# Kernel optimization log

Measured on AMD Instinct MI355X. Metric: run time of the kernel, lower is better.

The kernel has to match this reference:

```python
import jax, jax.numpy as jnp
import numpy as np

N = 50000      # nodes
E = 800000     # edges (before self-loops)
DIN = 128      # input feature dim
DOUT = 128     # per-head output dim
H = 4          # heads (concat=False -> mean over heads)
SLOPE = 0.2    # PyG GATConv default negative_slope


def setup_inputs() -> dict:
    key = jax.random.key(0)
    k1, k2, k3, k4, k5 = jax.random.split(key, 5)
    x = jax.random.normal(k1, (N, DIN), dtype=jnp.float32)
    edge_index = jax.random.randint(k2, (2, E), 0, N)
    W = jax.random.normal(k3, (DIN, H * DOUT), dtype=jnp.float32) / np.sqrt(DIN).astype(np.float32)
    att_src = jax.random.normal(k4, (H, DOUT), dtype=jnp.float32) * 0.1
    att_dst = jax.random.normal(k5, (H, DOUT), dtype=jnp.float32) * 0.1
    return {"x": x, "edge_index": edge_index, "W": W, "att_src": att_src, "att_dst": att_dst}


def _gat(x, W, att_src, att_dst, src, dst):
    h = (x @ W).reshape(N, H, DOUT)                      # [N,H,C] shared lin for src/dst
    a_s = jnp.einsum('nhc,hc->nh', h, att_src)           # [N,H]
    a_d = jnp.einsum('nhc,hc->nh', h, att_dst)           # [N,H]
    logits = jax.nn.leaky_relu(a_s[src] + a_d[dst], SLOPE)   # [Etot,H]
    m = jax.ops.segment_max(logits, dst, num_segments=N)     # segment softmax (stable)
    e = jnp.exp(logits - m[dst])
    denom = jax.ops.segment_sum(e, dst, num_segments=N)
    alpha = e / (denom[dst] + 1e-16)                         # [Etot,H]
    out = jax.ops.segment_sum(alpha[:, :, None] * h[src], dst, num_segments=N)  # [N,H,C]
    return out.mean(axis=1)                                   # concat=False -> average heads


def reference(x, edge_index, W, att_src, att_dst):
    loop = jnp.arange(N, dtype=edge_index.dtype)          # add_self_loops=True (PyG default)
    src = jnp.concatenate([edge_index[0], loop])
    dst = jnp.concatenate([edge_index[1], loop])
    return _gat(x, W, att_src, att_dst, src, dst)
```

## Files before the change

kernel.cpp:

```cpp
#include <hip/hip_runtime.h>

#define NN 50000
#define EE 800000
#define ETOT (EE + NN)
#define MAXD 96
#define NBK 196
#define CAP 6144
#define CHX 2304
#define TM 16

typedef _Float16 f16x8 __attribute__((ext_vector_type(8)));
typedef _Float16 f16x2 __attribute__((ext_vector_type(2)));
typedef float f32x4 __attribute__((ext_vector_type(4)));
typedef float f32x2 __attribute__((ext_vector_type(2)));
typedef unsigned int u32x4 __attribute__((ext_vector_type(4)));

__device__ __forceinline__ float lrelu(float v) { return v > 0.f ? v : 0.2f * v; }
__device__ __forceinline__ unsigned int pack2(float a, float b) {
  unsigned short lo = __builtin_bit_cast(unsigned short, (_Float16)a);
  unsigned short hi = __builtin_bit_cast(unsigned short, (_Float16)b);
  return (unsigned int)lo | ((unsigned int)hi << 16);
}

__global__ void k_prep(const float* __restrict__ W,
                       const float* __restrict__ att_s,
                       const float* __restrict__ att_d,
                       unsigned short* __restrict__ Bt,
                       float* __restrict__ WaS, float* __restrict__ WaD,
                       int* __restrict__ bcnt) {
  int gid = blockIdx.x * blockDim.x + threadIdx.x;
  if (gid < NBK) bcnt[gid] = 0;
  if (gid < 128 * 512) {
    int col = gid >> 9, k = gid & 511;
    float v = W[(k & 127) * 512 + (k >> 7) * 128 + col];
    _Float16 hv = (_Float16)v;
    Bt[col * 512 + k] = __builtin_bit_cast(unsigned short, hv);
  }
  if (gid < 512) {
    int k = gid >> 2, h = gid & 3;
    const float* wrow = W + k * 512 + h * 128;
    const float* as = att_s + h * 128;
    const float* ad = att_d + h * 128;
    float ss = 0.f, sd = 0.f;
    for (int c = 0; c < 128; ++c) { float w = wrow[c]; ss += w * as[c]; sd += w * ad[c]; }
    WaS[k * 4 + h] = ss;
    WaD[k * 4 + h] = sd;
  }
}

__global__ __launch_bounds__(256) void k_xcast_p1(const float* __restrict__ x,
                                                  const float* __restrict__ WaS,
                                                  const float* __restrict__ WaD,
                                                  const int* __restrict__ ei,
                                                  unsigned int* __restrict__ xh,
                                                  float* __restrict__ a_s,
                                                  float* __restrict__ a_d,
                                                  int* __restrict__ bcnt,
                                                  unsigned int* __restrict__ ebuf) {
  __shared__ unsigned long long D[128][33];
  __shared__ float4 wsl[128];
  __shared__ float4 wdl[128];
  __shared__ int cnt[NBK];
  __shared__ int gbase[NBK];
  int t = threadIdx.x;
  int nb = blockIdx.x * 128;
  if (t < 128) wsl[t] = ((const float4*)WaS)[t];
  else wdl[t - 128] = ((const float4*)WaD)[t - 128];
  for (int i = t; i < NBK; i += 256) cnt[i] = 0;

#pragma unroll
  for (int i = 0; i < 16; ++i) {
    int idx = t + i * 256;
    int n = idx >> 5, c4 = idx & 31;
    int gn = nb + n;
    float4 v = make_float4(0.f, 0.f, 0.f, 0.f);
    if (gn < NN) v = ((const float4*)x)[(size_t)gn * 32 + c4];
    unsigned int lo = pack2(v.x, v.y);
    unsigned int hi = pack2(v.z, v.w);
    if (gn < NN) ((uint2*)xh)[(size_t)gn * 32 + c4] = make_uint2(lo, hi);
    D[n][c4] = (unsigned long long)lo | ((unsigned long long)hi << 32);
  }
  __syncthreads();

  {
    int n = t >> 1, half = t & 1;
    float s0 = 0.f, s1 = 0.f, s2 = 0.f, s3 = 0.f;
    float d0 = 0.f, d1 = 0.f, d2 = 0.f, d3 = 0.f;
#pragma unroll
    for (int p = 0; p < 16; ++p) {
      int c4 = 2 * p + half;
      unsigned long long q = D[n][c4];
      f16x2 lo2 = __builtin_bit_cast(f16x2, (unsigned int)q);
      f16x2 hi2 = __builtin_bit_cast(f16x2, (unsigned int)(q >> 32));
      float f0 = (float)lo2[0], f1 = (float)lo2[1];
      float f2 = (float)hi2[0], f3 = (float)hi2[1];
      int c = c4 * 4;
      float4 w0 = wsl[c], w1 = wsl[c + 1], w2 = wsl[c + 2], w3 = wsl[c + 3];
      s0 += f0 * w0.x + f1 * w1.x + f2 * w2.x + f3 * w3.x;
      s1 += f0 * w0.y + f1 * w1.y + f2 * w2.y + f3 * w3.y;
      s2 += f0 * w0.z + f1 * w1.z + f2 * w2.z + f3 * w3.z;
      s3 += f0 * w0.w + f1 * w1.w + f2 * w2.w + f3 * w3.w;
      float4 v0 = wdl[c], v1 = wdl[c + 1], v2 = wdl[c + 2], v3 = wdl[c + 3];
      d0 += f0 * v0.x + f1 * v1.x + f2 * v2.x + f3 * v3.x;
      d1 += f0 * v0.y + f1 * v1.y + f2 * v2.y + f3 * v3.y;
      d2 += f0 * v0.z + f1 * v1.z + f2 * v2.z + f3 * v3.z;
      d3 += f0 * v0.w + f1 * v1.w + f2 * v2.w + f3 * v3.w;
    }
    s0 += __shfl_xor(s0, 1); s1 += __shfl_xor(s1, 1);
    s2 += __shfl_xor(s2, 1); s3 += __shfl_xor(s3, 1);
    d0 += __shfl_xor(d0, 1); d1 += __shfl_xor(d1, 1);
    d2 += __shfl_xor(d2, 1); d3 += __shfl_xor(d3, 1);
    int gn = nb + n;
    if (half == 0 && gn < NN) {
      *(float4*)(a_s + gn * 4) = make_float4(s0, s1, s2, s3);
      *(float4*)(a_d + gn * 4) = make_float4(d0, d1, d2, d3);
    }
  }

  int e0 = blockIdx.x * CHX;
#pragma unroll
  for (int k = 0; k < CHX / 256; ++k) {
    int e = e0 + t + k * 256;
    if (e < ETOT) {
      int d = (e < EE) ? ei[EE + e] : (e - EE);
      atomicAdd(&cnt[d >> 8], 1);
    }
  }
  __syncthreads();
  for (int i = t; i < NBK; i += 256) {
    gbase[i] = (cnt[i] > 0) ? atomicAdd(&bcnt[i], cnt[i]) : 0;
    cnt[i] = 0;
  }
  __syncthreads();
#pragma unroll
  for (int k = 0; k < CHX / 256; ++k) {
    int e = e0 + t + k * 256;
    if (e < ETOT) {
      int s, d;
      if (e < EE) { s = ei[e]; d = ei[EE + e]; } else { s = d = e - EE; }
      int b = d >> 8;
      int idx = gbase[b] + atomicAdd(&cnt[b], 1);
      if (idx < CAP)
        ebuf[(size_t)b * CAP + idx] = (unsigned int)s | ((unsigned int)(d & 255) << 16);
    }
  }
}

__global__ __launch_bounds__(256) void k_p2(const unsigned int* __restrict__ ebuf,
                                            const int* __restrict__ bcnt,
                                            int* __restrict__ rs,
                                            unsigned short* __restrict__ perm16) {
  __shared__ int sb[256];
  __shared__ int loc[256];
  __shared__ int cnt[256];
  __shared__ unsigned short out16[CAP];
  __shared__ int basesh;
  int b = blockIdx.x, t = threadIdx.x;

  int v = (t < NBK) ? bcnt[t] : 0;
  sb[t] = v;
  __syncthreads();
  for (int off = 1; off < 256; off <<= 1) {
    int u = (t >= off) ? sb[t - off] : 0;
    __syncthreads();
    sb[t] += u;
    __syncthreads();
  }
  if (t == b) basesh = sb[t] - v;
  cnt[t] = 0;
  __syncthreads();

  int base = basesh;
  int m = min(bcnt[b], CAP);
  int d0 = b * 256;
  const unsigned int* rec = ebuf + (size_t)b * CAP;
  for (int i = t; i < m; i += 256) atomicAdd(&cnt[rec[i] >> 16], 1);
  __syncthreads();

  int c = cnt[t];
  sb[t] = c;
  __syncthreads();
  for (int off = 1; off < 256; off <<= 1) {
    int u = (t >= off) ? sb[t - off] : 0;
    __syncthreads();
    sb[t] += u;
    __syncthreads();
  }
  int ex = sb[t] - c;
  loc[t] = ex;
  int gi = d0 + t;
  if (gi < NN) rs[gi] = base + ex;
  if (b == NBK - 1 && t == 0) rs[NN] = base + m;
  cnt[t] = 0;
  __syncthreads();

  for (int i = t; i < m; i += 256) {
    unsigned int r = rec[i];
    int dl = r >> 16;
    int rk = atomicAdd(&cnt[dl], 1);
    out16[loc[dl] + rk] = (unsigned short)(r & 0xffffu);
  }
  __syncthreads();
  for (int i = t; i < m; i += 256) perm16[base + i] = out16[i];
}

__global__ __launch_bounds__(256) void k_fused(const float* __restrict__ a_s,
                                               const float* __restrict__ a_d,
                                               const unsigned int* __restrict__ xh,
                                               const int* __restrict__ rs,
                                               const unsigned short* __restrict__ perm16,
                                               const unsigned short* __restrict__ Bt,
                                               float* __restrict__ out) {
  __shared__ u32x4 Zl[TM * 64];
  __shared__ float4 w_s[4][MAXD];
  __shared__ unsigned short sn_s[4][MAXD];
  unsigned int* Zw = (unsigned int*)Zl;
  int wave = threadIdx.x >> 6, lane = threadIdx.x & 63;
  int m0 = blockIdx.x * TM;

#pragma unroll 1
  for (int i = 0; i < 4; ++i) {
    int r = wave * 4 + i;
    int n = m0 + r;
    bool valid = (n < NN);
    int s = 0, deg = 0;
    float4 ad = make_float4(0.f, 0.f, 0.f, 0.f);
    if (valid) {
      s = rs[n];
      deg = rs[n + 1] - s;
      ad = *(const float4*)(a_d + n * 4);
    }
    bool fast = (deg <= MAXD);
    float t0 = 0.f, t1 = 0.f, t2 = 0.f, t3 = 0.f;
    if (fast) {
      for (int j = lane; j < deg; j += 64) {
        int sn = perm16[s + j];
        sn_s[wave][j] = (unsigned short)sn;
        float4 as = *(const float4*)(a_s + sn * 4);
        float e0 = __expf(lrelu(as.x + ad.x));
        float e1 = __expf(lrelu(as.y + ad.y));
        float e2 = __expf(lrelu(as.z + ad.z));
        float e3 = __expf(lrelu(as.w + ad.w));
        w_s[wave][j] = make_float4(e0, e1, e2, e3);
        t0 += e0; t1 += e1; t2 += e2; t3 += e3;
      }
    } else {
      for (int j = lane; j < deg; j += 64) {
        int sn = perm16[s + j];
        float4 as = *(const float4*)(a_s + sn * 4);
        t0 += __expf(lrelu(as.x + ad.x)); t1 += __expf(lrelu(as.y + ad.y));
        t2 += __expf(lrelu(as.z + ad.z)); t3 += __expf(lrelu(as.w + ad.w));
      }
    }
#pragma unroll
    for (int off = 32; off; off >>= 1) {
      t0 += __shfl_xor(t0, off); t1 += __shfl_xor(t1, off);
      t2 += __shfl_xor(t2, off); t3 += __shfl_xor(t3, off);
    }
    float sc0 = 0.25f / (t0 + 1e-16f), sc1 = 0.25f / (t1 + 1e-16f);
    float sc2 = 0.25f / (t2 + 1e-16f), sc3 = 0.25f / (t3 + 1e-16f);
    __builtin_amdgcn_wave_barrier();

    f32x2 za0 = {0.f, 0.f}, za1 = {0.f, 0.f}, za2 = {0.f, 0.f}, za3 = {0.f, 0.f};
    if (fast) {
      int j = 0;
      for (; j + 8 <= deg; j += 8) {
        unsigned int u[8];
        float4 w[8];
#pragma unroll
        for (int k = 0; k < 8; ++k) {
          int sa = sn_s[wave][j + k];
          u[k] = xh[sa * 64 + lane];
          w[k] = w_s[wave][j + k];
        }
#pragma unroll
        for (int k = 0; k < 8; ++k) {
          f16x2 p = __builtin_bit_cast(f16x2, u[k]);
          f32x2 xv = {(float)p[0], (float)p[1]};
          za0 += w[k].x * xv; za1 += w[k].y * xv;
          za2 += w[k].z * xv; za3 += w[k].w * xv;
        }
      }
      if (j + 4 <= deg) {
        unsigned int u[4];
        float4 w[4];
#pragma unroll
        for (int k = 0; k < 4; ++k) {
          int sa = sn_s[wave][j + k];
          u[k] = xh[sa * 64 + lane];
          w[k] = w_s[wave][j + k];
        }
#pragma unroll
        for (int k = 0; k < 4; ++k) {
          f16x2 p = __builtin_bit_cast(f16x2, u[k]);
          f32x2 xv = {(float)p[0], (float)p[1]};
          za0 += w[k].x * xv; za1 += w[k].y * xv;
          za2 += w[k].z * xv; za3 += w[k].w * xv;
        }
        j += 4;
      }
      for (; j < deg; ++j) {
        int sa = sn_s[wave][j];
        float4 w = w_s[wave][j];
        unsigned int u = xh[sa * 64 + lane];
        f16x2 p = __builtin_bit_cast(f16x2, u);
        f32x2 xv = {(float)p[0], (float)p[1]};
        za0 += w.x * xv; za1 += w.y * xv; za2 += w.z * xv; za3 += w.w * xv;
      }
    } else {
      for (int j = 0; j < deg; ++j) {
        int sn = perm16[s + j];
        float4 as = *(const float4*)(a_s + sn * 4);
        float w0 = __expf(lrelu(as.x + ad.x));
        float w1 = __expf(lrelu(as.y + ad.y));
        float w2 = __expf(lrelu(as.z + ad.z));
        float w3 = __expf(lrelu(as.w + ad.w));
        unsigned int u = xh[sn * 64 + lane];
        f16x2 p = __builtin_bit_cast(f16x2, u);
        f32x2 xv = {(float)p[0], (float)p[1]};
        za0 += w0 * xv; za1 += w1 * xv; za2 += w2 * xv; za3 += w3 * xv;
      }
    }

    unsigned int pk0 = pack2(za0[0] * sc0, za0[1] * sc0);
    unsigned int pk1 = pack2(za1[0] * sc1, za1[1] * sc1);
    unsigned int pk2 = pack2(za2[0] * sc2, za2[1] * sc2);
    unsigned int pk3 = pack2(za3[0] * sc3, za3[1] * sc3);
    if (!valid) { pk0 = 0u; pk1 = 0u; pk2 = 0u; pk3 = 0u; }
    int rb = r & 7;
    int ct = lane >> 2, sub = lane & 3;
    Zw[r * 256 + (((0 * 16 + ct) ^ rb) << 2) + sub] = pk0;
    Zw[r * 256 + (((1 * 16 + ct) ^ rb) << 2) + sub] = pk1;
    Zw[r * 256 + (((2 * 16 + ct) ^ rb) << 2) + sub] = pk2;
    Zw[r * 256 + (((3 * 16 + ct) ^ rb) << 2) + sub] = pk3;
  }
  __syncthreads();

  int lr = lane & 15, lk = lane >> 4;
  int n0w = wave * 32;
  const u32x4* Bv = (const u32x4*)Bt;
  f32x4 acc[2];
#pragma unroll
  for (int ni = 0; ni < 2; ++ni) acc[ni] = (f32x4){0.f, 0.f, 0.f, 0.f};

#pragma unroll
  for (int kk = 0; kk < 16; ++kk) {
    f16x8 af = __builtin_bit_cast(f16x8, Zl[lr * 64 + ((kk * 4 + lk) ^ (lr & 7))]);
#pragma unroll
    for (int ni = 0; ni < 2; ++ni) {
      int cix = n0w + ni * 16 + lr;
      f16x8 bf = __builtin_bit_cast(f16x8, Bv[cix * 64 + kk * 4 + lk]);
      acc[ni] = __builtin_amdgcn_mfma_f32_16x16x32_f16(af, bf, acc[ni], 0, 0, 0);
    }
  }

  int cr = lk * 4;
#pragma unroll
  for (int j2 = 0; j2 < 4; ++j2) {
    int row = m0 + cr + j2;
    if (row < NN) {
#pragma unroll
      for (int ni = 0; ni < 2; ++ni) {
        int col = n0w + ni * 16 + lr;
        out[row * 128 + col] = acc[ni][j2];
      }
    }
  }
}

extern "C" void kernel_launch(void* const* d_in, const int* in_sizes, int n_in,
                              void* d_out, int out_size, void* d_ws, size_t ws_size,
                              hipStream_t stream) {
  const float* x = (const float*)d_in[0];
  const int* ei = (const int*)d_in[1];
  const float* W = (const float*)d_in[2];
  const float* att_s = (const float*)d_in[3];
  const float* att_d = (const float*)d_in[4];
  float* out = (float*)d_out;
  char* ws = (char*)d_ws;

  unsigned int* xh = (unsigned int*)(ws + 0);
  unsigned int* ebuf = (unsigned int*)(ws + 12800000);
  unsigned short* Bt = (unsigned short*)(ws + 17616896);
  float* WaS = (float*)(ws + 17747968);
  float* WaD = (float*)(ws + 17750016);
  float* a_s = (float*)(ws + 17752064);
  float* a_d = (float*)(ws + 18552064);
  int* rs = (int*)(ws + 19352064);
  int* bcnt = (int*)(ws + 19552256);
  unsigned short* perm16 = (unsigned short*)(ws + 19553280);

  k_prep<<<256, 256, 0, stream>>>(W, att_s, att_d, Bt, WaS, WaD, bcnt);
  k_xcast_p1<<<(NN + 127) / 128, 256, 0, stream>>>(x, WaS, WaD, ei, xh, a_s, a_d, bcnt, ebuf);
  k_p2<<<NBK, 256, 0, stream>>>(ebuf, bcnt, rs, perm16);
  k_fused<<<(NN + TM - 1) / TM, 256, 0, stream>>>(a_s, a_d, xh, rs, perm16, Bt, out);
}
```

Before: 145.5 us.

## Assign one wave per destination node with 1024-thread blocks in fused GAT kernel

The fused aggregation kernel now launches 1024-thread blocks where each of 16 waves handles a single destination node, replacing the loop in which 4 waves each processed 4 nodes serially. The first-pass weight computation becomes a single predicated step per lane (MAXD lowered to 64), and the per-edge weights are stored as two f32x2 arrays. Only 8 waves then run the MFMA projection, each producing 16 output columns. This aims to expose more memory-level parallelism for the gather, at the cost of idle waves during the matmul and more nodes falling back to the slow path when degree exceeds 64. Bounds checks on n are dropped, which relies on NN being a multiple of 16.

```diff
diff --git a/kernel.cpp b/kernel.cpp
--- a/kernel.cpp
+++ b/kernel.cpp
@@ -3,7 +3,7 @@
 #define NN 50000
 #define EE 800000
 #define ETOT (EE + NN)
-#define MAXD 96
+#define MAXD 64
 #define NBK 196
 #define CAP 6144
 #define CHX 2304
@@ -204,167 +204,142 @@
   for (int i = t; i < m; i += 256) perm16[base + i] = out16[i];
 }
 
-__global__ __launch_bounds__(256) void k_fused(const float* __restrict__ a_s,
-                                               const float* __restrict__ a_d,
-                                               const unsigned int* __restrict__ xh,
-                                               const int* __restrict__ rs,
-                                               const unsigned short* __restrict__ perm16,
-                                               const unsigned short* __restrict__ Bt,
-                                               float* __restrict__ out) {
+__global__ __launch_bounds__(1024, 2) void k_fused(const float* __restrict__ a_s,
+                                                   const float* __restrict__ a_d,
+                                                   const unsigned int* __restrict__ xh,
+                                                   const int* __restrict__ rs,
+                                                   const unsigned short* __restrict__ perm16,
+                                                   const unsigned short* __restrict__ Bt,
+                                                   float* __restrict__ out) {
   __shared__ u32x4 Zl[TM * 64];
-  __shared__ float4 w_s[4][MAXD];
-  __shared__ unsigned short sn_s[4][MAXD];
+  __shared__ f32x2 wlo[16][MAXD];
+  __shared__ f32x2 whi[16][MAXD];
+  __shared__ unsigned short sn_s[16][MAXD];
   unsigned int* Zw = (unsigned int*)Zl;
   int wave = threadIdx.x >> 6, lane = threadIdx.x & 63;
   int m0 = blockIdx.x * TM;
-
-#pragma unroll 1
-  for (int i = 0; i < 4; ++i) {
-    int r = wave * 4 + i;
-    int n = m0 + r;
-    bool valid = (n < NN);
-    int s = 0, deg = 0;
-    float4 ad = make_float4(0.f, 0.f, 0.f, 0.f);
-    if (valid) {
-      s = rs[n];
-      deg = rs[n + 1] - s;
-      ad = *(const float4*)(a_d + n * 4);
-    }
-    bool fast = (deg <= MAXD);
-    float t0 = 0.f, t1 = 0.f, t2 = 0.f, t3 = 0.f;
-    if (fast) {
-      for (int j = lane; j < deg; j += 64) {
-        int sn = perm16[s + j];
-        sn_s[wave][j] = (unsigned short)sn;
-        float4 as = *(const float4*)(a_s + sn * 4);
-        float e0 = __expf(lrelu(as.x + ad.x));
-        float e1 = __expf(lrelu(as.y + ad.y));
-        float e2 = __expf(lrelu(as.z + ad.z));
-        float e3 = __expf(lrelu(as.w + ad.w));
-        w_s[wave][j] = make_float4(e0, e1, e2, e3);
-        t0 += e0; t1 += e1; t2 += e2; t3 += e3;
+  int n = m0 + wave;
+
+  int s = rs[n];
+  int deg = rs[n + 1] - s;
+  float4 ad = *(const float4*)(a_d + n * 4);
+  bool fast = (deg <= MAXD);
+
+  float t0 = 0.f, t1 = 0.f, t2 = 0.f, t3 = 0.f;
+  if (fast) {
+    if (lane < deg) {
+      int sn = perm16[s + lane];
+      sn_s[wave][lane] = (unsigned short)sn;
+      float4 as = *(const float4*)(a_s + sn * 4);
+      float e0 = __expf(lrelu(as.x + ad.x));
+      float e1 = __expf(lrelu(as.y + ad.y));
+      float e2 = __expf(lrelu(as.z + ad.z));
+      float e3 = __expf(lrelu(as.w + ad.w));
+      wlo[wave][lane] = (f32x2){e0, e1};
+      whi[wave][lane] = (f32x2){e2, e3};
+      t0 = e0; t1 = e1; t2 = e2; t3 = e3;
+    }
+  } else {
+    for (int j = lane; j < deg; j += 64) {
+      int sn = perm16[s + j];
+      float4 as = *(const float4*)(a_s + sn * 4);
+      t0 += __expf(lrelu(as.x + ad.x)); t1 += __expf(lrelu(as.y + ad.y));
+      t2 += __expf(lrelu(as.z + ad.z)); t3 += __expf(lrelu(as.w + ad.w));
+    }
+  }
+#pragma unroll
+  for (int off = 32; off; off >>= 1) {
+    t0 += __shfl_xor(t0, off); t1 += __shfl_xor(t1, off);
+    t2 += __shfl_xor(t2, off); t3 += __shfl_xor(t3, off);
+  }
+  float sc0 = 0.25f / (t0 + 1e-16f), sc1 = 0.25f / (t1 + 1e-16f);
+  float sc2 = 0.25f / (t2 + 1e-16f), sc3 = 0.25f / (t3 + 1e-16f);
+  __builtin_amdgcn_wave_barrier();
+
+  f32x2 za0 = {0.f, 0.f}, za1 = {0.f, 0.f}, za2 = {0.f, 0.f}, za3 = {0.f, 0.f};
+  if (fast) {
+    int j = 0;
+    for (; j + 8 <= deg; j += 8) {
+      unsigned int u[8];
+#pragma unroll
+      for (int k = 0; k < 8; ++k) u[k] = xh[(int)sn_s[wave][j + k] * 64 + lane];
+#pragma unroll
+      for (int k = 0; k < 8; ++k) {
+        f32x2 wl = wlo[wave][j + k];
+        f32x2 wh = whi[wave][j + k];
+        f16x2 p = __builtin_bit_cast(f16x2, u[k]);
+        f32x2 xv = {(float)p[0], (float)p[1]};
+        za0 += wl[0] * xv; za1 += wl[1] * xv;
+        za2 += wh[0] * xv; za3 += wh[1] * xv;
       }
-    } else {
-      for (int j = lane; j < deg; j += 64) {
-        int sn = perm16[s + j];
-        float4 as = *(const float4*)(a_s + sn * 4);
-        t0 += __expf(lrelu(as.x + ad.x)); t1 += __expf(lrelu(as.y + ad.y));
-        t2 += __expf(lrelu(as.z + ad.z)); t3 += __expf(lrelu(as.w + ad.w));
+    }
+    if (j + 4 <= deg) {
+      unsigned int u[4];
+#pragma unroll
+      for (int k = 0; k < 4; ++k) u[k] = xh[(int)sn_s[wave][j + k] * 64 + lane];
+#pragma unroll
+      for (int k = 0; k < 4; ++k) {
+        f32x2 wl = wlo[wave][j + k];
+        f32x2 wh = whi[wave][j + k];
+        f16x2 p = __builtin_bit_cast(f16x2, u[k]);
+        f32x2 xv = {(float)p[0], (float)p[1]};
+        za0 += wl[0] * xv; za1 += wl[1] * xv;
+        za2 += wh[0] * xv; za3 += wh[1] * xv;
       }
-    }
-#pragma unroll
-    for (int off = 32; off; off >>= 1) {
-      t0 += __shfl_xor(t0, off); t1 += __shfl_xor(t1, off);
-      t2 += __shfl_xor(t2, off); t3 += __shfl_xor(t3, off);
-    }
-    float sc0 = 0.25f / (t0 + 1e-16f), sc1 = 0.25f / (t1 + 1e-16f);
-    float sc2 = 0.25f / (t2 + 1e-16f), sc3 = 0.25f / (t3 + 1e-16f);
-    __builtin_amdgcn_wave_barrier();
-
-    f32x2 za0 = {0.f, 0.f}, za1 = {0.f, 0.f}, za2 = {0.f, 0.f}, za3 = {0.f, 0.f};
-    if (fast) {
-      int j = 0;
-      for (; j + 8 <= deg; j += 8) {
-        unsigned int u[8];
-        float4 w[8];
-#pragma unroll
-        for (int k = 0; k < 8; ++k) {
-          int sa = sn_s[wave][j + k];
-          u[k] = xh[sa * 64 + lane];
-          w[k] = w_s[wave][j + k];
-        }
-#pragma unroll
-        for (int k = 0; k < 8; ++k) {
-          f16x2 p = __builtin_bit_cast(f16x2, u[k]);
-          f32x2 xv = {(float)p[0], (float)p[1]};
-          za0 += w[k].x * xv; za1 += w[k].y * xv;
-          za2 += w[k].z * xv; za3 += w[k].w * xv;
-        }
-      }
-      if (j + 4 <= deg) {
-        unsigned int u[4];
-        float4 w[4];
-#pragma unroll
-        for (int k = 0; k < 4; ++k) {
-          int sa = sn_s[wave][j + k];
-          u[k] = xh[sa * 64 + lane];
-          w[k] = w_s[wave][j + k];
-        }
-#pragma unroll
-        for (int k = 0; k < 4; ++k) {
-          f16x2 p = __builtin_bit_cast(f16x2, u[k]);
-          f32x2 xv = {(float)p[0], (float)p[1]};
-          za0 += w[k].x * xv; za1 += w[k].y * xv;
-          za2 += w[k].z * xv; za3 += w[k].w * xv;
-        }
-        j += 4;
-      }
-      for (; j < deg; ++j) {
-        int sa = sn_s[wave][j];
-        float4 w = w_s[wave][j];
-        unsigned int u = xh[sa * 64 + lane];
-        f16x2 p = __builtin_bit_cast(f16x2, u);
-        f32x2 xv = {(float)p[0], (float)p[1]};
-        za0 += w.x * xv; za1 += w.y * xv; za2 += w.z * xv; za3 += w.w * xv;
-      }
-    } else {
-      for (int j = 0; j < deg; ++j) {
-        int sn = perm16[s + j];
-        float4 as = *(const float4*)(a_s + sn * 4);
-        float w0 = __expf(lrelu(as.x + ad.x));
-        float w1 = __expf(lrelu(as.y + ad.y));
-        float w2 = __expf(lrelu(as.z + ad.z));
-        float w3 = __expf(lrelu(as.w + ad.w));
-        unsigned int u = xh[sn * 64 + lane];
-        f16x2 p = __builtin_bit_cast(f16x2, u);
-        f32x2 xv = {(float)p[0], (float)p[1]};
-        za0 += w0 * xv; za1 += w1 * xv; za2 += w2 * xv; za3 += w3 * xv;
-      }
-    }
-
-    unsigned int pk0 = pack2(za0[0] * sc0, za0[1] * sc0);
-    unsigned int pk1 = pack2(za1[0] * sc1, za1[1] * sc1);
-    unsigned int pk2 = pack2(za2[0] * sc2, za2[1] * sc2);
-    unsigned int pk3 = pack2(za3[0] * sc3, za3[1] * sc3);
-    if (!valid) { pk0 = 0u; pk1 = 0u; pk2 = 0u; pk3 = 0u; }
-    int rb = r & 7;
-    int ct = lane >> 2, sub = lane & 3;
-    Zw[r * 256 + (((0 * 16 + ct) ^ rb) << 2) + sub] = pk0;
-    Zw[r * 256 + (((1 * 16 + ct) ^ rb) << 2) + sub] = pk1;
-    Zw[r * 256 + (((2 * 16 + ct) ^ rb) << 2) + sub] = pk2;
-    Zw[r * 256 + (((3 * 16 + ct) ^ rb) << 2) + sub] = pk3;
-  }
-  __syncthreads();
+      j += 4;
+    }
+    for (; j < deg; ++j) {
+      f32x2 wl = wlo[wave][j];
+      f32x2 wh = whi[wave][j];
+      unsigned int u = xh[(int)sn_s[wave][j] * 64 + lane];
+      f16x2 p = __builtin_bit_cast(f16x2, u);
+      f32x2 xv = {(float)p[0], (float)p[1]};
+      za0 += wl[0] * xv; za1 += wl[1] * xv;
+      za2 += wh[0] * xv; za3 += wh[1] * xv;
+    }
+  } else {
+    for (int j = 0; j < deg; ++j) {
+      int sn = perm16[s + j];
+      float4 as = *(const float4*)(a_s + sn * 4);
+      float w0 = __expf(lrelu(as.x + ad.x));
+      float w1 = __expf(lrelu(as.y + ad.y));
+      float w2 = __expf(lrelu(as.z + ad.z));
+      float w3 = __expf(lrelu(as.w + ad.w));
+      unsigned int u = xh[sn * 64 + lane];
+      f16x2 p = __builtin_bit_cast(f16x2, u);
+      f32x2 xv = {(float)p[0], (float)p[1]};
+      za0 += w0 * xv; za1 += w1 * xv; za2 += w2 * xv; za3 += w3 * xv;
+    }
+  }
+
+  unsigned int pk0 = pack2(za0[0] * sc0, za0[1] * sc0);
+  unsigned int pk1 = pack2(za1[0] * sc1, za1[1] * sc1);
+  unsigned int pk2 = pack2(za2[0] * sc2, za2[1] * sc2);
+  unsigned int pk3 = pack2(za3[0] * sc3, za3[1] * sc3);
+  int rb = wave & 7;
+  int ct = lane >> 2, sub = lane & 3;
+  Zw[wave * 256 + (((0 * 16 + ct) ^ rb) << 2) + sub] = pk0;
+  Zw[wave * 256 + (((1 * 16 + ct) ^ rb) << 2) + sub] = pk1;
+  Zw[wave * 256 + (((2 * 16 + ct) ^ rb) << 2) + sub] = pk2;
+  Zw[wave * 256 + (((3 * 16 + ct) ^ rb) << 2) + sub] = pk3;
+  __syncthreads();
+
+  if (wave >= 8) return;
 
   int lr = lane & 15, lk = lane >> 4;
-  int n0w = wave * 32;
+  int n0w = wave * 16;
   const u32x4* Bv = (const u32x4*)Bt;
-  f32x4 acc[2];
-#pragma unroll
-  for (int ni = 0; ni < 2; ++ni) acc[ni] = (f32x4){0.f, 0.f, 0.f, 0.f};
-
+  f32x4 acc = (f32x4){0.f, 0.f, 0.f, 0.f};
 #pragma unroll
   for (int kk = 0; kk < 16; ++kk) {
     f16x8 af = __builtin_bit_cast(f16x8, Zl[lr * 64 + ((kk * 4 + lk) ^ (lr & 7))]);
-#pragma unroll
-    for (int ni = 0; ni < 2; ++ni) {
-      int cix = n0w + ni * 16 + lr;
-      f16x8 bf = __builtin_bit_cast(f16x8, Bv[cix * 64 + kk * 4 + lk]);
-      acc[ni] = __builtin_amdgcn_mfma_f32_16x16x32_f16(af, bf, acc[ni], 0, 0, 0);
-    }
-  }
-
+    f16x8 bf = __builtin_bit_cast(f16x8, Bv[(n0w + lr) * 64 + kk * 4 + lk]);
+    acc = __builtin_amdgcn_mfma_f32_16x16x32_f16(af, bf, acc, 0, 0, 0);
+  }
   int cr = lk * 4;
 #pragma unroll
   for (int j2 = 0; j2 < 4; ++j2) {
-    int row = m0 + cr + j2;
-    if (row < NN) {
-#pragma unroll
-      for (int ni = 0; ni < 2; ++ni) {
-        int col = n0w + ni * 16 + lr;
-        out[row * 128 + col] = acc[ni][j2];
-      }
-    }
+    out[(m0 + cr + j2) * 128 + n0w + lr] = acc[j2];
   }
 }
 
@@ -393,5 +368,5 @@
   k_prep<<<256, 256, 0, stream>>>(W, att_s, att_d, Bt, WaS, WaD, bcnt);
   k_xcast_p1<<<(NN + 127) / 128, 256, 0, stream>>>(x, WaS, WaD, ei, xh, a_s, a_d, bcnt, ebuf);
   k_p2<<<NBK, 256, 0, stream>>>(ebuf, bcnt, rs, perm16);
-  k_fused<<<(NN + TM - 1) / TM, 256, 0, stream>>>(a_s, a_d, xh, rs, perm16, Bt, out);
-}
+  k_fused<<<NN / TM, 1024, 0, stream>>>(a_s, a_d, xh, rs, perm16, Bt, out);
+}
```

Result: faster. 139.0 us (-4.5%).
